# Performance work log

Hardware: AMD Instinct MI355X
Metric: run time of the kernel (lower is better)

## Reference

```python
import jax, jax.numpy as jnp
import numpy as np

POOL_H, POOL_W = 7, 7


def _crop_and_resize(fm, boxes, ph, pw):
    """tf.image.crop_and_resize (bilinear) for all boxes in all batch images.

    fm: [B, H, W, C] feature map; boxes: [B, N, 4] as (y1, x1, y2, x2) in
    normalized coords. Returns [B, N, ph, pw, C].
    """
    B, H, W, C = fm.shape
    y1, x1, y2, x2 = boxes[..., 0], boxes[..., 1], boxes[..., 2], boxes[..., 3]
    ty = jnp.arange(ph, dtype=fm.dtype) / (ph - 1)               # [ph]
    tx = jnp.arange(pw, dtype=fm.dtype) / (pw - 1)               # [pw]
    # in_y = y1*(H-1) + i*(y2-y1)*(H-1)/(ph-1)  (TF crop_and_resize, crop>1)
    ys = (y1[..., None] + (y2 - y1)[..., None] * ty) * (H - 1)   # [B,N,ph]
    xs = (x1[..., None] + (x2 - x1)[..., None] * tx) * (W - 1)   # [B,N,pw]
    y0f = jnp.floor(ys)
    x0f = jnp.floor(xs)
    wy = (ys - y0f)[:, :, :, None, None]                         # [B,N,ph,1,1]
    wx = (xs - x0f)[:, :, None, :, None]                         # [B,N,1,pw,1]
    y0 = jnp.clip(y0f.astype(jnp.int32), 0, H - 1)
    y1i = jnp.clip(y0 + 1, 0, H - 1)
    x0 = jnp.clip(x0f.astype(jnp.int32), 0, W - 1)
    x1i = jnp.clip(x0 + 1, 0, W - 1)
    b = jnp.arange(B)[:, None, None, None]                        # [B,1,1,1]
    yA = y0[:, :, :, None]
    yB = y1i[:, :, :, None]                                       # [B,N,ph,1]
    xA = x0[:, :, None, :]
    xB = x1i[:, :, None, :]                                       # [B,N,1,pw]
    v00 = fm[b, yA, xA]                                           # [B,N,ph,pw,C]
    v01 = fm[b, yA, xB]
    v10 = fm[b, yB, xA]
    v11 = fm[b, yB, xB]
    top = v00 + (v01 - v00) * wx
    bot = v10 + (v11 - v10) * wx
    return top + (bot - top) * wy


def _roi_levels(boxes, image_shape):
    """FPN level assignment: clip(4 + round(log2(sqrt(h*w)*sqrt(area)/224)), 2, 5)."""
    h = boxes[..., 2] - boxes[..., 0]
    w = boxes[..., 3] - boxes[..., 1]
    image_area = (image_shape[0] * image_shape[1]).astype(jnp.float32)
    scaled_area = jnp.sqrt(h * w) * jnp.sqrt(image_area) / 224.0
    lvl = 4 + jnp.round(jnp.log2(scaled_area)).astype(jnp.int32)
    return jnp.clip(lvl, 2, 5)                                    # [B,N]


def setup_inputs():
    key = jax.random.key(0)
    kb, k2, k3, k4, k5 = jax.random.split(key, 5)
    B, N, C = 2, 1000, 256
    # valid boxes: y1 <= y2, x1 <= x2, generically nonzero area
    r = jax.random.uniform(kb, (B, N, 2, 2), dtype=jnp.float32)
    boxes = jnp.concatenate([r.min(axis=2), r.max(axis=2)], axis=-1)
    image_shape = jnp.array([1024, 1024], dtype=jnp.int32)
    p2 = jax.random.normal(k2, (B, 256, 256, C), dtype=jnp.float32)
    p3 = jax.random.normal(k3, (B, 128, 128, C), dtype=jnp.float32)
    p4 = jax.random.normal(k4, (B, 64, 64, C), dtype=jnp.float32)
    p5 = jax.random.normal(k5, (B, 32, 32, C), dtype=jnp.float32)
    return {"boxes": boxes, "image_shape": image_shape,
            "p2": p2, "p3": p3, "p4": p4, "p5": p5}


def reference(boxes, image_shape, p2, p3, p4, p5):
    # The TF layer routes each box to one pyramid level, crops there, then
    # sorts pooled features back into (batch, box) order. That composite is
    # mathematically: for each box, crop_and_resize from its assigned level.
    lvl = _roi_levels(boxes, image_shape)                         # [B,N] in {2..5}
    crop_boxes = jax.lax.stop_gradient(boxes)                     # TF stop_gradient
    pooled_all = jnp.stack(
        [_crop_and_resize(fm, crop_boxes, POOL_H, POOL_W)
         for fm in (p2, p3, p4, p5)], axis=0)                     # [4,B,N,ph,pw,C]
    idx = (lvl - 2)[None, :, :, None, None, None].astype(jnp.int32)
    idx = jnp.broadcast_to(idx, (1,) + pooled_all.shape[1:])
    return jnp.take_along_axis(pooled_all, idx, axis=0)[0]        # [B,N,ph,pw,C]
```

## Files before the change

### kernel.cpp

```cpp
#include <hip/hip_runtime.h>
#include <cmath>

#define NPOS 49

__global__ __launch_bounds__(256) void roi_align_kernel(
    const float* __restrict__ boxes,
    const int*   __restrict__ image_shape,
    const float* __restrict__ p2,
    const float* __restrict__ p3,
    const float* __restrict__ p4,
    const float* __restrict__ p5,
    float* __restrict__ out,
    int N, int C, int H2)
{
    const int bn = blockIdx.x;
    const int b  = bn / N;

    const float* bx = boxes + (size_t)bn * 4;
    const float y1 = bx[0], x1 = bx[1], y2 = bx[2], x2 = bx[3];
    const float h = y2 - y1, w = x2 - x1;

    const float img_area = (float)(image_shape[0] * image_shape[1]);
    const float scaled = sqrtf(h * w) * sqrtf(img_area) / 224.0f;
    int lvl = 4 + (int)rintf(log2f(scaled));
    lvl = min(5, max(2, lvl));

    const float* fm;
    int H;
    switch (lvl) {
        case 2:  fm = p2; H = H2;      break;
        case 3:  fm = p3; H = H2 >> 1; break;
        case 4:  fm = p4; H = H2 >> 2; break;
        default: fm = p5; H = H2 >> 3; break;
    }
    const int W = H;

    const int tid = threadIdx.x;
    const int cg  = tid & 63;
    const int wv  = tid >> 6;
    const int c   = cg * 4;

    const float Hm1 = (float)(H - 1);
    const float Wm1 = (float)(W - 1);
    const float inv6 = 1.0f / 6.0f;

    const float* fmb = fm + (size_t)b * H * W * C;
    float* outp = out + (size_t)bn * NPOS * C + c;

    for (int pos = wv; pos < NPOS; pos += 4) {
        const int py = pos / 7;
        const int px = pos - py * 7;

        const float ys = (y1 + h * ((float)py * inv6)) * Hm1;
        const float xs = (x1 + w * ((float)px * inv6)) * Wm1;
        const float y0f = floorf(ys), x0f = floorf(xs);
        const float wy = ys - y0f;
        const float wx = xs - x0f;
        int y0 = (int)y0f; y0 = min(H - 1, max(0, y0));
        int x0 = (int)x0f; x0 = min(W - 1, max(0, x0));
        const int yb = min(H - 1, y0 + 1);
        const int xb = min(W - 1, x0 + 1);

        const float* r0 = fmb + ((size_t)y0 * W) * C;
        const float* r1 = fmb + ((size_t)yb * W) * C;

        const float4 v00 = *(const float4*)(r0 + (size_t)x0 * C + c);
        const float4 v01 = *(const float4*)(r0 + (size_t)xb * C + c);
        const float4 v10 = *(const float4*)(r1 + (size_t)x0 * C + c);
        const float4 v11 = *(const float4*)(r1 + (size_t)xb * C + c);

        float4 res;
        {
            float top, bot;
            top = v00.x + (v01.x - v00.x) * wx;
            bot = v10.x + (v11.x - v10.x) * wx;
            res.x = top + (bot - top) * wy;
            top = v00.y + (v01.y - v00.y) * wx;
            bot = v10.y + (v11.y - v10.y) * wx;
            res.y = top + (bot - top) * wy;
            top = v00.z + (v01.z - v00.z) * wx;
            bot = v10.z + (v11.z - v10.z) * wx;
            res.z = top + (bot - top) * wy;
            top = v00.w + (v01.w - v00.w) * wx;
            bot = v10.w + (v11.w - v10.w) * wx;
            res.w = top + (bot - top) * wy;
        }

        *(float4*)(outp + (size_t)pos * C) = res;
    }
}

extern "C" void kernel_launch(void* const* d_in, const int* in_sizes, int n_in,
                              void* d_out, int out_size, void* d_ws, size_t ws_size,
                              hipStream_t stream) {
    const float* boxes       = (const float*)d_in[0];
    const int*   image_shape = (const int*)d_in[1];
    const float* p2          = (const float*)d_in[2];
    const float* p3          = (const float*)d_in[3];
    const float* p4          = (const float*)d_in[4];
    const float* p5          = (const float*)d_in[5];
    float* out = (float*)d_out;

    const int B  = 2;
    const int BN = in_sizes[0] / 4;
    const int N  = BN / B;
    const int C  = out_size / (BN * NPOS);
    const int H2 = (int)llround(sqrt((double)in_sizes[2] / ((double)B * C)));

    roi_align_kernel<<<BN, 256, 0, stream>>>(boxes, image_shape, p2, p3, p4, p5,
                                             out, N, C, H2);
}
```

Before: 258.7 us.

## Map one wavefront per (box, sample position) and use nontemporal stores

Each wavefront now handles a single (box, pooled position) pair, in place of a block looping over all 49 positions. This removes the tail imbalance in which one of four waves does 13 iterations and the others 12, and it raises the number of blocks so more loads are in flight. Output writes use nontemporal vector stores so the streamed result does not pollute cache. The cost is that box and level setup is repeated for every position, 49 times per box.

```diff
diff --git a/kernel.cpp b/kernel.cpp
--- a/kernel.cpp
+++ b/kernel.cpp
@@ -2,6 +2,8 @@
 #include <cmath>
 
 #define NPOS 49
+
+typedef float nfloat4 __attribute__((ext_vector_type(4)));
 
 __global__ __launch_bounds__(256) void roi_align_kernel(
     const float* __restrict__ boxes,
@@ -11,10 +13,14 @@
     const float* __restrict__ p4,
     const float* __restrict__ p5,
     float* __restrict__ out,
-    int N, int C, int H2)
+    int N, int C, int H2, int BN)
 {
-    const int bn = blockIdx.x;
-    const int b  = bn / N;
+    const int gw  = blockIdx.x * 4 + (threadIdx.x >> 6);
+    const int bn  = gw / NPOS;
+    const int pos = gw - bn * NPOS;
+    if (bn >= BN) return;
+
+    const int b = bn / N;
 
     const float* bx = boxes + (size_t)bn * 4;
     const float y1 = bx[0], x1 = bx[1], y2 = bx[2], x2 = bx[3];
@@ -35,59 +41,40 @@
     }
     const int W = H;
 
-    const int tid = threadIdx.x;
-    const int cg  = tid & 63;
-    const int wv  = tid >> 6;
-    const int c   = cg * 4;
+    const int c = (threadIdx.x & 63) * 4;
 
     const float Hm1 = (float)(H - 1);
     const float Wm1 = (float)(W - 1);
     const float inv6 = 1.0f / 6.0f;
 
+    const int py = pos / 7;
+    const int px = pos - py * 7;
+
+    const float ys = (y1 + h * ((float)py * inv6)) * Hm1;
+    const float xs = (x1 + w * ((float)px * inv6)) * Wm1;
+    const float y0f = floorf(ys), x0f = floorf(xs);
+    const float wy = ys - y0f;
+    const float wx = xs - x0f;
+    int y0 = (int)y0f; y0 = min(H - 1, max(0, y0));
+    int x0 = (int)x0f; x0 = min(W - 1, max(0, x0));
+    const int yb = min(H - 1, y0 + 1);
+    const int xb = min(W - 1, x0 + 1);
+
     const float* fmb = fm + (size_t)b * H * W * C;
-    float* outp = out + (size_t)bn * NPOS * C + c;
+    const float* r0 = fmb + ((size_t)y0 * W) * C;
+    const float* r1 = fmb + ((size_t)yb * W) * C;
 
-    for (int pos = wv; pos < NPOS; pos += 4) {
-        const int py = pos / 7;
-        const int px = pos - py * 7;
+    const nfloat4 v00 = *(const nfloat4*)(r0 + (size_t)x0 * C + c);
+    const nfloat4 v01 = *(const nfloat4*)(r0 + (size_t)xb * C + c);
+    const nfloat4 v10 = *(const nfloat4*)(r1 + (size_t)x0 * C + c);
+    const nfloat4 v11 = *(const nfloat4*)(r1 + (size_t)xb * C + c);
 
-        const float ys = (y1 + h * ((float)py * inv6)) * Hm1;
-        const float xs = (x1 + w * ((float)px * inv6)) * Wm1;
-        const float y0f = floorf(ys), x0f = floorf(xs);
-        const float wy = ys - y0f;
-        const float wx = xs - x0f;
-        int y0 = (int)y0f; y0 = min(H - 1, max(0, y0));
-        int x0 = (int)x0f; x0 = min(W - 1, max(0, x0));
-        const int yb = min(H - 1, y0 + 1);
-        const int xb = min(W - 1, x0 + 1);
+    const nfloat4 top = v00 + (v01 - v00) * wx;
+    const nfloat4 bot = v10 + (v11 - v10) * wx;
+    const nfloat4 res = top + (bot - top) * wy;
 
-        const float* r0 = fmb + ((size_t)y0 * W) * C;
-        const float* r1 = fmb + ((size_t)yb * W) * C;
-
-        const float4 v00 = *(const float4*)(r0 + (size_t)x0 * C + c);
-        const float4 v01 = *(const float4*)(r0 + (size_t)xb * C + c);
-        const float4 v10 = *(const float4*)(r1 + (size_t)x0 * C + c);
-        const float4 v11 = *(const float4*)(r1 + (size_t)xb * C + c);
-
-        float4 res;
-        {
-            float top, bot;
-            top = v00.x + (v01.x - v00.x) * wx;
-            bot = v10.x + (v11.x - v10.x) * wx;
-            res.x = top + (bot - top) * wy;
-            top = v00.y + (v01.y - v00.y) * wx;
-            bot = v10.y + (v11.y - v10.y) * wx;
-            res.y = top + (bot - top) * wy;
-            top = v00.z + (v01.z - v00.z) * wx;
-            bot = v10.z + (v11.z - v10.z) * wx;
-            res.z = top + (bot - top) * wy;
-            top = v00.w + (v01.w - v00.w) * wx;
-            bot = v10.w + (v11.w - v10.w) * wx;
-            res.w = top + (bot - top) * wy;
-        }
-
-        *(float4*)(outp + (size_t)pos * C) = res;
-    }
+    nfloat4* dst = (nfloat4*)(out + (size_t)bn * NPOS * C + (size_t)pos * C + c);
+    __builtin_nontemporal_store(res, dst);
 }
 
 extern "C" void kernel_launch(void* const* d_in, const int* in_sizes, int n_in,
@@ -107,6 +94,8 @@
     const int C  = out_size / (BN * NPOS);
     const int H2 = (int)llround(sqrt((double)in_sizes[2] / ((double)B * C)));
 
-    roi_align_kernel<<<BN, 256, 0, stream>>>(boxes, image_shape, p2, p3, p4, p5,
-                                             out, N, C, H2);
+    const int total_waves = BN * NPOS;
+    const int grid = (total_waves + 3) / 4;
+    roi_align_kernel<<<grid, 256, 0, stream>>>(boxes, image_shape, p2, p3, p4, p5,
+                                               out, N, C, H2, BN);
 }
```

New measurement: 248.0 us. 4.1% less time.
